# Optimization experiments

Measured on AMD Instinct MI355X. Metric: run time of the kernel, lower is better.

Reference implementation:

```python
import jax, jax.numpy as jnp
import numpy as np

N = 50000      # nodes
E = 800000     # edges
IN = 128       # input feature dim
HID = 64       # out_channels per head
HEADS = 2
OUT = 40       # num classes
SLOPE = 0.2    # leaky relu negative slope
EPS = 1e-16    # PyG softmax denominator epsilon


def _xavier(key, shape):
    fan_out, fan_in = shape[0], shape[1]
    a = float(np.sqrt(6.0 / (fan_in + fan_out)))
    return jax.random.uniform(key, shape, minval=-a, maxval=a, dtype=jnp.float32)


def setup_inputs() -> dict:
    key = jax.random.key(0)
    ks = jax.random.split(key, 16)
    x = jax.random.normal(ks[0], (N, IN), dtype=jnp.float32)
    edge_index = jax.random.randint(ks[1], (2, E), 0, N, dtype=jnp.int64)
    # GAT layer 1: lin_l == lin_r (shared), weight [H*C, in], att [C, H]
    W1 = _xavier(ks[2], (HEADS * HID, IN))
    b1 = jnp.zeros((HEADS * HID,), jnp.float32)
    al1 = _xavier(ks[3], (HID, HEADS))
    ar1 = _xavier(ks[4], (HID, HEADS))
    # GAT layer 2: input dim = heads*hidden
    W2 = _xavier(ks[5], (HEADS * HID, HEADS * HID))
    b2 = jnp.zeros((HEADS * HID,), jnp.float32)
    al2 = _xavier(ks[6], (HID, HEADS))
    ar2 = _xavier(ks[7], (HID, HEADS))
    # post_mp: Linear(heads*hid, hid) -> Linear(hid, out)
    Wp1 = _xavier(ks[8], (HID, HEADS * HID))
    bp1 = jnp.zeros((HID,), jnp.float32)
    Wp2 = _xavier(ks[9], (OUT, HID))
    bp2 = jnp.zeros((OUT,), jnp.float32)
    return dict(x=x, edge_index=edge_index, W1=W1, b1=b1, al1=al1, ar1=ar1,
                W2=W2, b2=b2, al2=al2, ar2=ar2, Wp1=Wp1, bp1=bp1, Wp2=Wp2, bp2=bp2)


def gat_layer(x, edge_index, W, b, att_l, att_r):
    """One GAT layer: shared linear, per-edge leaky-relu scores,
    segment-softmax keyed by destination node, scatter-sum."""
    n = x.shape[0]
    xt = (x @ W.T + b).reshape(n, HEADS, HID)          # [N, H, C] (x_l == x_r)
    alpha_l = jnp.einsum('nhc,ch->nh', xt, att_l)      # [N, H]
    alpha_r = jnp.einsum('nhc,ch->nh', xt, att_r)      # [N, H]
    src, dst = edge_index[0], edge_index[1]            # j = source, i = dest
    e = jax.nn.leaky_relu(alpha_r[dst] + alpha_l[src], SLOPE)   # [E, H]
    # segment softmax over edges grouped by destination node
    seg_max = jax.ops.segment_max(e, dst, num_segments=n)       # [N, H]
    ex = jnp.exp(e - seg_max[dst])
    denom = jax.ops.segment_sum(ex, dst, num_segments=n)        # [N, H]
    alpha = ex / (denom[dst] + EPS)                              # [E, H]
    msg = alpha[:, :, None] * xt[src]                            # [E, H, C]
    out = jax.ops.segment_sum(msg, dst, num_segments=n)          # [N, H, C]
    return out.reshape(n, HEADS * HID)


def reference(x, edge_index, W1, b1, al1, ar1, W2, b2, al2, ar2, Wp1, bp1, Wp2, bp2):
    h = jax.nn.relu(gat_layer(x, edge_index, W1, b1, al1, ar1))
    h = jax.nn.relu(gat_layer(h, edge_index, W2, b2, al2, ar2))
    h = h @ Wp1.T + bp1
    h = h @ Wp2.T + bp2
    return jax.nn.log_softmax(h, axis=1)
```

## Files before the change

kernel.cpp:

```cpp
#include <hip/hip_runtime.h>
#include <hip/hip_fp16.h>
#include <cmath>

#define N_NODES 50000
#define N_EDGES 800000
#define F 128
#define OUT_DIM 40
#define SLOPE 0.2f
#define EPS_DEN 1e-16f

#define BK_SHIFT 7
#define BKSZ 128
#define NBK ((N_NODES + BKSZ - 1) / BKSZ)
#define BK_CAP2 2560
#define SC_CHUNK 2500
#define SC_BLOCKS ((N_EDGES + SC_CHUNK - 1) / SC_CHUNK)
#define GEMM_TILES ((N_NODES + 127) / 128)
#define CB_BLOCKS 33
#define A_BLOCKS (SC_BLOCKS + CB_BLOCKS + GEMM_TILES)
#define SMEM_BYTES 21504
#define POISON ((int)0xAAAAAAAA)

#define AGG_TILE 32
#define AGG_TILES ((N_NODES + AGG_TILE - 1) / AGG_TILE)

typedef _Float16 half8 __attribute__((ext_vector_type(8)));
typedef float floatx4 __attribute__((ext_vector_type(4)));

struct ScatterS { int sd[SC_CHUNK]; short sb[SC_CHUNK]; int h[NBK]; int lofs[NBK]; };
struct GemmS    { __half Ah[128][40]; __half Bh[128][40]; };
static_assert(sizeof(ScatterS) <= SMEM_BYTES, "scatter LDS");
static_assert(sizeof(GemmS)    <= SMEM_BYTES, "gemm LDS");

__device__ __forceinline__ int swz(int row, int chunk) {
  return row * 128 + ((chunk ^ (row & 15)) << 3);
}

__device__ inline float4 load4(const float* p) { return *(const float4*)p; }
__device__ inline float4 load4(const __half* p) {
  uint2 u = *(const uint2*)p;
  float2 a = __half22float2(*(__half2*)&u.x);
  float2 b = __half22float2(*(__half2*)&u.y);
  return make_float4(a.x, a.y, b.x, b.y);
}

__device__ __forceinline__ void scatter_phase(const int* __restrict__ ei,
    int* __restrict__ bcur, int* __restrict__ pairs, int it, int tid, char* smem_) {
  ScatterS* S = (ScatterS*)smem_;
  for (int i = tid; i < NBK; i += 256) S->h[i] = 0;
  __syncthreads();
  int base = it * SC_CHUNK;
  int end = base + SC_CHUNK; if (end > N_EDGES) end = N_EDGES;
  int cnt = end - base;
  for (int e = base + tid; e < end; e += 256) {
    int s = ei[e];
    int d = ei[N_EDGES + e];
    int b = d >> BK_SHIFT;
    S->sd[e - base] = (s << BK_SHIFT) | (d & (BKSZ - 1));
    S->sb[e - base] = (short)b;
    atomicAdd(&S->h[b], 1);
  }
  __syncthreads();
  for (int i = tid; i < NBK; i += 256)
    if (S->h[i]) {
      S->lofs[i] = i * BK_CAP2 + (atomicAdd(&bcur[i], S->h[i]) - POISON);
      S->h[i] = 0;
    }
  __syncthreads();
  for (int i = tid; i < cnt; i += 256) {
    int b = S->sb[i];
    int pos = S->lofs[b] + atomicAdd(&S->h[b], 1);
    pairs[pos] = S->sd[i];
  }
}

__device__ __forceinline__ void combine_phase(const float* __restrict__ Wp1,
    const float* __restrict__ bp1, const float* __restrict__ Wp2,
    const float* __restrict__ bp2, const float* __restrict__ W2,
    __half* __restrict__ Wch, float* __restrict__ bc,
    __half* __restrict__ W2h, int it, int tid) {
  if (it < 24) {
    int idx = it * 256 + tid;
    int o = idx >> 7, k = idx & 127;
    float s = 0.f;
    if (o < OUT_DIM) {
#pragma unroll 8
      for (int j = 0; j < 64; ++j) s += Wp2[o * 64 + j] * Wp1[j * 128 + k];
    }
    Wch[o * 128 + k] = __float2half(s);
  } else if (it == 24) {
    if (tid < 48) {
      int o = tid;
      if (o < OUT_DIM) {
        float s = bp2[o];
        for (int j = 0; j < 64; ++j) s += Wp2[o * 64 + j] * bp1[j];
        bc[o] = s;
      } else {
        bc[o] = -1e30f;
      }
    }
  } else {
    int idx = (it - 25) * 2048 + tid * 8;
    const float* q = W2 + idx;
    float4 w0 = *(const float4*)q, w1 = *(const float4*)(q + 4);
    __half2 g0 = __floats2half2_rn(w0.x, w0.y), g1 = __floats2half2_rn(w0.z, w0.w);
    __half2 g2 = __floats2half2_rn(w1.x, w1.y), g3 = __floats2half2_rn(w1.z, w1.w);
    uint4 qk; qk.x = *(unsigned*)&g0; qk.y = *(unsigned*)&g1;
    qk.z = *(unsigned*)&g2; qk.w = *(unsigned*)&g3;
    *(uint4*)&W2h[idx] = qk;
  }
}

template <typename T>
__device__ __forceinline__ void gemm_phase(const T* __restrict__ A,
    const float* __restrict__ W, const float* __restrict__ b,
    const float* __restrict__ attl, const float* __restrict__ attr,
    __half* __restrict__ Ch, float* __restrict__ al, float* __restrict__ ar,
    int nrows, int tile, int tid, char* smem_) {
  GemmS* S = (GemmS*)smem_;
  int lane = tid & 63, wid = tid >> 6;
  int quad = lane >> 4, col = lane & 15;
  int r0 = tile * 128;
  int rowhalf = wid >> 1, colhalf = wid & 1;
  floatx4 acc[4][4] = {};
  for (int kc = 0; kc < 128; kc += 32) {
    for (int i = tid; i < 512; i += 256) {
      int row = i >> 2, seg = i & 3;
      int gr = r0 + row;
      float4 v0, v1;
      if (gr < nrows) {
        const T* p = A + (size_t)gr * 128 + kc + seg * 8;
        v0 = load4(p); v1 = load4(p + 4);
      } else { v0 = make_float4(0.f,0.f,0.f,0.f); v1 = v0; }
      __half2 h0 = __floats2half2_rn(v0.x, v0.y), h1 = __floats2half2_rn(v0.z, v0.w);
      __half2 h2 = __floats2half2_rn(v1.x, v1.y), h3 = __floats2half2_rn(v1.z, v1.w);
      uint4 pk; pk.x = *(unsigned*)&h0; pk.y = *(unsigned*)&h1;
      pk.z = *(unsigned*)&h2; pk.w = *(unsigned*)&h3;
      *(uint4*)&S->Ah[row][seg * 8] = pk;
      const float* q = W + (size_t)row * 128 + kc + seg * 8;
      float4 w0 = *(const float4*)q, w1 = *(const float4*)(q + 4);
      __half2 g0 = __floats2half2_rn(w0.x, w0.y), g1 = __floats2half2_rn(w0.z, w0.w);
      __half2 g2 = __floats2half2_rn(w1.x, w1.y), g3 = __floats2half2_rn(w1.z, w1.w);
      uint4 qk; qk.x = *(unsigned*)&g0; qk.y = *(unsigned*)&g1;
      qk.z = *(unsigned*)&g2; qk.w = *(unsigned*)&g3;
      *(uint4*)&S->Bh[row][seg * 8] = qk;
    }
    __syncthreads();
    half8 afr[4], bfr[4];
#pragma unroll
    for (int rt = 0; rt < 4; ++rt)
      afr[rt] = *(const half8*)&S->Ah[rowhalf * 64 + rt * 16 + col][quad * 8];
#pragma unroll
    for (int ct = 0; ct < 4; ++ct)
      bfr[ct] = *(const half8*)&S->Bh[colhalf * 64 + ct * 16 + col][quad * 8];
#pragma unroll
    for (int rt = 0; rt < 4; ++rt)
#pragma unroll
      for (int ct = 0; ct < 4; ++ct)
        acc[rt][ct] = __builtin_amdgcn_mfma_f32_16x16x32_f16(afr[rt], bfr[ct],
                                                             acc[rt][ct], 0, 0, 0);
    __syncthreads();
  }
  int head = colhalf;
  float bj[4], wl4[4], wr4[4];
#pragma unroll
  for (int ct = 0; ct < 4; ++ct) {
    int c = ct * 16 + col;
    bj[ct] = b[head * 64 + c];
    wl4[ct] = attl[c * 2 + head];
    wr4[ct] = attr[c * 2 + head];
  }
#pragma unroll
  for (int rt = 0; rt < 4; ++rt) {
#pragma unroll
    for (int reg = 0; reg < 4; ++reg) {
      int gr = r0 + rowhalf * 64 + rt * 16 + quad * 4 + reg;
      bool ok = gr < nrows;
      float pl = 0.f, pr = 0.f;
#pragma unroll
      for (int ct = 0; ct < 4; ++ct) {
        float v = acc[rt][ct][reg] + bj[ct];
        pl += v * wl4[ct]; pr += v * wr4[ct];
        if (ok) Ch[(size_t)gr * F + head * 64 + ct * 16 + col] = __float2half(v);
      }
      pl += __shfl_xor(pl, 1, 64); pr += __shfl_xor(pr, 1, 64);
      pl += __shfl_xor(pl, 2, 64); pr += __shfl_xor(pr, 2, 64);
      pl += __shfl_xor(pl, 4, 64); pr += __shfl_xor(pr, 4, 64);
      pl += __shfl_xor(pl, 8, 64); pr += __shfl_xor(pr, 8, 64);
      if (ok && col == 0) { al[gr * 2 + head] = pl; ar[gr * 2 + head] = pr; }
    }
  }
}

__global__ __launch_bounds__(256) void kernelA(const int* __restrict__ ei,
    int* __restrict__ bcur, int* __restrict__ pairs,
    const float* __restrict__ Wp1, const float* __restrict__ bp1,
    const float* __restrict__ Wp2, const float* __restrict__ bp2,
    const float* __restrict__ W2, __half* __restrict__ Wch,
    float* __restrict__ bc, __half* __restrict__ W2h,
    const float* __restrict__ x, const float* __restrict__ W1,
    const float* __restrict__ b1, const float* __restrict__ al1,
    const float* __restrict__ ar1, __half* __restrict__ xh,
    float* __restrict__ al, float* __restrict__ ar) {
  __shared__ __align__(16) char smem[SMEM_BYTES];
  int bid = blockIdx.x, tid = threadIdx.x;
  if (bid < SC_BLOCKS) {
    scatter_phase(ei, bcur, pairs, bid, tid, smem);
  } else if (bid < SC_BLOCKS + CB_BLOCKS) {
    combine_phase(Wp1, bp1, Wp2, bp2, W2, Wch, bc, W2h, bid - SC_BLOCKS, tid);
  } else {
    gemm_phase<float>(x, W1, b1, al1, ar1, xh, al, ar, N_NODES,
                      bid - SC_BLOCKS - CB_BLOCKS, tid, smem);
  }
}

__global__ __launch_bounds__(512) void local_sort(const int* __restrict__ bcur,
    const int* __restrict__ pairs, int* __restrict__ rowstart,
    int* __restrict__ rowend, int* __restrict__ srcs) {
  __shared__ int buf[BK_CAP2];
  __shared__ int sorted[BK_CAP2];
  __shared__ int hist[BKSZ];
  __shared__ int cur[BKSZ];
  int tid = threadIdx.x;
  int b = blockIdx.x;
  int base = b * BK_CAP2;
  int cnt = bcur[b] - POISON;
  if (cnt > BK_CAP2) cnt = BK_CAP2;
  if (cnt < 0) cnt = 0;
  if (tid < BKSZ) hist[tid] = 0;
  __syncthreads();
  for (int i = tid; i < cnt; i += 512) {
    int p = pairs[base + i];
    buf[i] = p;
    atomicAdd(&hist[p & (BKSZ - 1)], 1);
  }
  __syncthreads();
  if (tid < 64) {
    int lane = tid;
    int carry = 0;
#pragma unroll
    for (int c = 0; c < BKSZ; c += 64) {
      int v = hist[c + lane];
      int x = v;
#pragma unroll
      for (int off = 1; off < 64; off <<= 1) {
        int t = __shfl_up(x, off, 64);
        if (lane >= off) x += t;
      }
      int excl = carry + x - v;
      cur[c + lane] = excl;
      int node = b * BKSZ + c + lane;
      if (node < N_NODES) {
        rowstart[node] = base + excl;
        rowend[node]   = base + excl + v;
      }
      carry += __shfl(x, 63, 64);
    }
  }
  __syncthreads();
  for (int i = tid; i < cnt; i += 512) {
    int p = buf[i];
    int pos = atomicAdd(&cur[p & (BKSZ - 1)], 1);
    sorted[pos] = p >> BK_SHIFT;
  }
  __syncthreads();
  for (int i = tid; i < cnt; i += 512)
    srcs[base + i] = sorted[i];
}

__device__ __forceinline__ void agg_node_to_lds(const int* __restrict__ rowstart,
    const int* __restrict__ rowend, const int* __restrict__ srcs,
    const float* __restrict__ al, const float* __restrict__ ar,
    const __half* __restrict__ xsrc, __half* __restrict__ ldsA,
    float (*ebufw)[64], int* sbufw, int node, int ldsrow, int lane) {
  int g = lane >> 4, q = lane & 15;
  int head = q >> 3;
  if (node >= N_NODES) {
    if (g == 0) {
      uint4 z = {0, 0, 0, 0};
      *(uint4*)&ldsA[swz(ldsrow, q)] = z;
    }
    __builtin_amdgcn_wave_barrier();
    return;
  }
  int start = rowstart[node], end = rowend[node];
  float2 arv = *(const float2*)(ar + (size_t)node * 2);
  float ar0 = arv.x, ar1 = arv.y;
  const float* wrow = &ebufw[head][0];
  const __half* xbase = xsrc + q * 8;
  float acc[8] = {};
  float dl0 = 0.f, dl1 = 0.f;
  for (int c = start; c < end; c += 64) {
    int j = c + lane;
    float e0 = 0.f, e1 = 0.f; int soff = 0;
    if (j < end) {
      int s = srcs[j];
      soff = s << BK_SHIFT;
      float2 a = *(const float2*)(al + (size_t)s * 2);
      float s0 = a.x + ar0; s0 = (s0 > 0.f) ? s0 : SLOPE * s0;
      float s1 = a.y + ar1; s1 = (s1 > 0.f) ? s1 : SLOPE * s1;
      e0 = __expf(s0); e1 = __expf(s1);
    }
    dl0 += e0; dl1 += e1;
    ebufw[0][lane] = e0; ebufw[1][lane] = e1; sbufw[lane] = soff;
    __builtin_amdgcn_wave_barrier();
    int cend = end - c; if (cend > 64) cend = 64;
#pragma unroll 4
    for (int t = 0; t < cend; t += 4) {
      int te = t + g;
      if (te < cend) {
        int so = sbufw[te];
        float w = wrow[te];
        uint4 u = *(const uint4*)(xbase + so);
        const __half2* hh = (const __half2*)&u;
        float2 f0 = __half22float2(hh[0]);
        float2 f1 = __half22float2(hh[1]);
        float2 f2 = __half22float2(hh[2]);
        float2 f3 = __half22float2(hh[3]);
        acc[0] += w * f0.x; acc[1] += w * f0.y;
        acc[2] += w * f1.x; acc[3] += w * f1.y;
        acc[4] += w * f2.x; acc[5] += w * f2.y;
        acc[6] += w * f3.x; acc[7] += w * f3.y;
      }
    }
    __builtin_amdgcn_wave_barrier();
  }
#pragma unroll
  for (int off = 32; off > 0; off >>= 1) {
    dl0 += __shfl_xor(dl0, off, 64);
    dl1 += __shfl_xor(dl1, off, 64);
  }
#pragma unroll
  for (int k = 0; k < 8; ++k) {
    acc[k] += __shfl_xor(acc[k], 16, 64);
    acc[k] += __shfl_xor(acc[k], 32, 64);
  }
  if (g == 0) {
    float d = (head == 0) ? dl0 : dl1;
    float inv = 1.f / (d + EPS_DEN);
    __half2 o0 = __floats2half2_rn(fmaxf(acc[0] * inv, 0.f), fmaxf(acc[1] * inv, 0.f));
    __half2 o1 = __floats2half2_rn(fmaxf(acc[2] * inv, 0.f), fmaxf(acc[3] * inv, 0.f));
    __half2 o2 = __floats2half2_rn(fmaxf(acc[4] * inv, 0.f), fmaxf(acc[5] * inv, 0.f));
    __half2 o3 = __floats2half2_rn(fmaxf(acc[6] * inv, 0.f), fmaxf(acc[7] * inv, 0.f));
    uint4 pack;
    pack.x = *(unsigned*)&o0; pack.y = *(unsigned*)&o1;
    pack.z = *(unsigned*)&o2; pack.w = *(unsigned*)&o3;
    *(uint4*)&ldsA[swz(ldsrow, q)] = pack;
  }
  __builtin_amdgcn_wave_barrier();
}

__global__ __launch_bounds__(256) void fusedB(const int* __restrict__ rowstart,
    const int* __restrict__ rowend, const int* __restrict__ srcs,
    const float* __restrict__ al, const float* __restrict__ ar,
    const __half* __restrict__ xh, const __half* __restrict__ W2h,
    const float* __restrict__ b2,
    const float* __restrict__ attl, const float* __restrict__ attr,
    __half* __restrict__ xh2, float* __restrict__ al2, float* __restrict__ ar2) {
  __shared__ __half Ah[AGG_TILE * 128];
  __shared__ float ebuf[4][2][64];
  __shared__ int   sbuf[4][64];
  int tid = threadIdx.x;
  int wid = tid >> 6, lane = tid & 63;
  int tile = blockIdx.x;
#pragma unroll 1
  for (int r = 0; r < 8; ++r) {
    int ldsrow = r * 4 + wid;
    agg_node_to_lds(rowstart, rowend, srcs, al, ar, xh, Ah,
                    ebuf[wid], sbuf[wid], tile * AGG_TILE + ldsrow, ldsrow, lane);
  }
  __syncthreads();
  int rowg = wid >> 1, colg = wid & 1;
  int quad = lane >> 4, col = lane & 15;
  floatx4 acc[4] = {};
#pragma unroll
  for (int kc4 = 0; kc4 < 4; ++kc4) {
    half8 afr = *(const half8*)&Ah[swz(rowg * 16 + col, (kc4 << 2) | quad)];
#pragma unroll
    for (int ct = 0; ct < 4; ++ct) {
      int brow = colg * 64 + ct * 16 + col;
      half8 bfr = *(const half8*)(W2h + (size_t)brow * 128 + kc4 * 32 + quad * 8);
      acc[ct] = __builtin_amdgcn_mfma_f32_16x16x32_f16(afr, bfr, acc[ct], 0, 0, 0);
    }
  }
  int head = colg;
  float bj[4], wl4[4], wr4[4];
#pragma unroll
  for (int ct = 0; ct < 4; ++ct) {
    int c = ct * 16 + col;
    bj[ct] = b2[head * 64 + c];
    wl4[ct] = attl[c * 2 + head];
    wr4[ct] = attr[c * 2 + head];
  }
#pragma unroll
  for (int reg = 0; reg < 4; ++reg) {
    int gr = tile * AGG_TILE + rowg * 16 + quad * 4 + reg;
    bool ok = gr < N_NODES;
    float pl = 0.f, pr = 0.f;
#pragma unroll
    for (int ct = 0; ct < 4; ++ct) {
      float v = acc[ct][reg] + bj[ct];
      pl += v * wl4[ct]; pr += v * wr4[ct];
      if (ok) xh2[(size_t)gr * F + head * 64 + ct * 16 + col] = __float2half(v);
    }
    pl += __shfl_xor(pl, 1, 64); pr += __shfl_xor(pr, 1, 64);
    pl += __shfl_xor(pl, 2, 64); pr += __shfl_xor(pr, 2, 64);
    pl += __shfl_xor(pl, 4, 64); pr += __shfl_xor(pr, 4, 64);
    pl += __shfl_xor(pl, 8, 64); pr += __shfl_xor(pr, 8, 64);
    if (ok && col == 0) { al2[gr * 2 + head] = pl; ar2[gr * 2 + head] = pr; }
  }
}

__global__ __launch_bounds__(256) void fusedC(const int* __restrict__ rowstart,
    const int* __restrict__ rowend, const int* __restrict__ srcs,
    const float* __restrict__ al2, const float* __restrict__ ar2,
    const __half* __restrict__ xh2,
    const __half* __restrict__ Wch, const float* __restrict__ bc,
    float* __restrict__ out) {
  __shared__ __half Ah[AGG_TILE * 128];
  __shared__ float ebuf[4][2][64];
  __shared__ int   sbuf[4][64];
  int tid = threadIdx.x;
  int wid = tid >> 6, lane = tid & 63;
  int tile = blockIdx.x;
#pragma unroll 1
  for (int r = 0; r < 8; ++r) {
    int ldsrow = r * 4 + wid;
    agg_node_to_lds(rowstart, rowend, srcs, al2, ar2, xh2, Ah,
                    ebuf[wid], sbuf[wid], tile * AGG_TILE + ldsrow, ldsrow, lane);
  }
  __syncthreads();
  if (wid >= 2) return;
  int quad = lane >> 4, col = lane & 15;
  int rbase = wid * 16;
  floatx4 acc[3] = {};
#pragma unroll
  for (int kc4 = 0; kc4 < 4; ++kc4) {
    half8 afr = *(const half8*)&Ah[swz(rbase + col, (kc4 << 2) | quad)];
#pragma unroll
    for (int ct = 0; ct < 3; ++ct) {
      half8 bfr = *(const half8*)(Wch + (size_t)(ct * 16 + col) * 128 + kc4 * 32 + quad * 8);
      acc[ct] = __builtin_amdgcn_mfma_f32_16x16x32_f16(afr, bfr, acc[ct], 0, 0, 0);
    }
  }
  float bcv[3];
#pragma unroll
  for (int ct = 0; ct < 3; ++ct) bcv[ct] = bc[ct * 16 + col];
#pragma unroll
  for (int reg = 0; reg < 4; ++reg) {
    int row = tile * AGG_TILE + rbase + quad * 4 + reg;
    float z[3], m = -INFINITY;
#pragma unroll
    for (int ct = 0; ct < 3; ++ct) { z[ct] = acc[ct][reg] + bcv[ct]; m = fmaxf(m, z[ct]); }
    m = fmaxf(m, __shfl_xor(m, 1, 64));
    m = fmaxf(m, __shfl_xor(m, 2, 64));
    m = fmaxf(m, __shfl_xor(m, 4, 64));
    m = fmaxf(m, __shfl_xor(m, 8, 64));
    float s = 0.f;
#pragma unroll
    for (int ct = 0; ct < 3; ++ct) s += __expf(z[ct] - m);
    s += __shfl_xor(s, 1, 64);
    s += __shfl_xor(s, 2, 64);
    s += __shfl_xor(s, 4, 64);
    s += __shfl_xor(s, 8, 64);
    float ls = logf(s);
    if (row < N_NODES) {
#pragma unroll
      for (int ct = 0; ct < 3; ++ct) {
        int o = ct * 16 + col;
        if (o < OUT_DIM) out[(size_t)row * OUT_DIM + o] = z[ct] - m - ls;
      }
    }
  }
}

extern "C" void kernel_launch(void* const* d_in, const int* in_sizes, int n_in,
                              void* d_out, int out_size, void* d_ws, size_t ws_size,
                              hipStream_t stream) {
  const float* x   = (const float*)d_in[0];
  const int*   ei  = (const int*)d_in[1];
  const float* W1  = (const float*)d_in[2];
  const float* b1  = (const float*)d_in[3];
  const float* al1 = (const float*)d_in[4];
  const float* ar1 = (const float*)d_in[5];
  const float* W2  = (const float*)d_in[6];
  const float* b2  = (const float*)d_in[7];
  const float* al2w= (const float*)d_in[8];
  const float* ar2w= (const float*)d_in[9];
  const float* Wp1 = (const float*)d_in[10];
  const float* bp1 = (const float*)d_in[11];
  const float* Wp2 = (const float*)d_in[12];
  const float* bp2 = (const float*)d_in[13];
  float* out = (float*)d_out;

  float* al    = (float*)d_ws;
  float* ar    = al + (size_t)N_NODES * 2;
  float* al2   = ar + (size_t)N_NODES * 2;
  float* ar2   = al2 + (size_t)N_NODES * 2;
  __half* Wch  = (__half*)(ar2 + (size_t)N_NODES * 2);
  float* bc    = (float*)(Wch + 48 * 128);
  __half* W2h  = (__half*)(bc + 48);
  int* rowstart= (int*)(W2h + 128 * 128);
  int* rowend  = rowstart + N_NODES;
  int* bcur    = rowend + N_NODES;
  int* srcs    = bcur + NBK;
  int* pairs   = srcs + NBK * BK_CAP2;
  uintptr_t pp = ((uintptr_t)(pairs + NBK * BK_CAP2) + 255) & ~(uintptr_t)255;
  __half* xh   = (__half*)pp;
  __half* xh2  = xh + (size_t)N_NODES * F;

  kernelA<<<A_BLOCKS, 256, 0, stream>>>(ei, bcur, pairs, Wp1, bp1, Wp2, bp2,
                                        W2, Wch, bc, W2h, x, W1, b1, al1, ar1,
                                        xh, al, ar);
  local_sort<<<NBK, 512, 0, stream>>>(bcur, pairs, rowstart, rowend, srcs);
  fusedB<<<AGG_TILES, 256, 0, stream>>>(rowstart, rowend, srcs, al, ar, xh,
                                        W2h, b2, al2w, ar2w, xh2, al2, ar2);
  fusedC<<<AGG_TILES, 256, 0, stream>>>(rowstart, rowend, srcs, al2, ar2, xh2,
                                        Wch, bc, out);
}
```

Before: 256.5 us.

## Aggregate per 128-node bucket with precomputed normalized edge weights in LDS

fusedB and fusedC now run one 1024-thread block per 128-node bucket instead of one 256-thread block per 32 nodes. Each block first computes the leaky-relu exp scores for all of the bucket's edges, the per-node softmax denominators and the normalized weights, and keeps them in LDS. To support this, local_sort now stores the packed (src, dst-low) value so the destination can be recovered per edge. The per-node gather then just reads weights and offsets from LDS, which removes the per-chunk wave barriers and the per-wave exp work. In exchange the grid is much smaller with heavier blocks, each block uses far more LDS, and the prologue adds block-wide syncs and a serial per-node denominator loop.

```diff
diff --git a/kernel.cpp b/kernel.cpp
--- a/kernel.cpp
+++ b/kernel.cpp
@@ -20,9 +20,6 @@
 #define A_BLOCKS (SC_BLOCKS + CB_BLOCKS + GEMM_TILES)
 #define SMEM_BYTES 21504
 #define POISON ((int)0xAAAAAAAA)
-
-#define AGG_TILE 32
-#define AGG_TILES ((N_NODES + AGG_TILE - 1) / AGG_TILE)
 
 typedef _Float16 half8 __attribute__((ext_vector_type(8)));
 typedef float floatx4 __attribute__((ext_vector_type(4)));
@@ -261,18 +258,59 @@
   for (int i = tid; i < cnt; i += 512) {
     int p = buf[i];
     int pos = atomicAdd(&cur[p & (BKSZ - 1)], 1);
-    sorted[pos] = p >> BK_SHIFT;
+    sorted[pos] = p;
   }
   __syncthreads();
   for (int i = tid; i < cnt; i += 512)
     srcs[base + i] = sorted[i];
 }
 
-__device__ __forceinline__ void agg_node_to_lds(const int* __restrict__ rowstart,
-    const int* __restrict__ rowend, const int* __restrict__ srcs,
+__device__ __forceinline__ void edge_softmax_prologue(
+    const int* __restrict__ rowstart, const int* __restrict__ rowend,
+    const int* __restrict__ srcs, const int* __restrict__ bcur,
     const float* __restrict__ al, const float* __restrict__ ar,
-    const __half* __restrict__ xsrc, __half* __restrict__ ldsA,
-    float (*ebufw)[64], int* sbufw, int node, int ldsrow, int lane) {
+    float2* __restrict__ wbuf, int* __restrict__ sofs,
+    unsigned char* __restrict__ dlo, float2* __restrict__ inv,
+    int tile, int tid) {
+  int base = tile * BK_CAP2;
+  int cnt = bcur[tile] - POISON;
+  if (cnt > BK_CAP2) cnt = BK_CAP2;
+  if (cnt < 0) cnt = 0;
+  for (int i = tid; i < cnt; i += 1024) {
+    int v = srcs[base + i];
+    int s = v >> BK_SHIFT;
+    int d = v & (BKSZ - 1);
+    sofs[i] = s << BK_SHIFT;
+    dlo[i] = (unsigned char)d;
+    float2 a = *(const float2*)(al + (size_t)s * 2);
+    float2 rr = *(const float2*)(ar + (size_t)(tile * BKSZ + d) * 2);
+    float s0 = a.x + rr.x; s0 = (s0 > 0.f) ? s0 : SLOPE * s0;
+    float s1 = a.y + rr.y; s1 = (s1 > 0.f) ? s1 : SLOPE * s1;
+    wbuf[i] = make_float2(__expf(s0), __expf(s1));
+  }
+  __syncthreads();
+  if (tid < BKSZ) {
+    int node = tile * BKSZ + tid;
+    float d0 = 0.f, d1 = 0.f;
+    if (node < N_NODES) {
+      int ls = rowstart[node] - base, le = rowend[node] - base;
+      for (int j = ls; j < le; ++j) { float2 w = wbuf[j]; d0 += w.x; d1 += w.y; }
+    }
+    inv[tid] = make_float2(1.f / (d0 + EPS_DEN), 1.f / (d1 + EPS_DEN));
+  }
+  __syncthreads();
+  for (int i = tid; i < cnt; i += 1024) {
+    float2 iv = inv[dlo[i]];
+    float2 w = wbuf[i];
+    wbuf[i] = make_float2(w.x * iv.x, w.y * iv.y);
+  }
+  __syncthreads();
+}
+
+__device__ __forceinline__ void agg_node(const int* __restrict__ rowstart,
+    const int* __restrict__ rowend, const __half* __restrict__ xsrc,
+    const float2* __restrict__ wbuf, const int* __restrict__ sofs,
+    __half* __restrict__ ldsA, int base, int node, int ldsrow, int lane) {
   int g = lane >> 4, q = lane & 15;
   int head = q >> 3;
   if (node >= N_NODES) {
@@ -280,55 +318,26 @@
       uint4 z = {0, 0, 0, 0};
       *(uint4*)&ldsA[swz(ldsrow, q)] = z;
     }
-    __builtin_amdgcn_wave_barrier();
     return;
   }
-  int start = rowstart[node], end = rowend[node];
-  float2 arv = *(const float2*)(ar + (size_t)node * 2);
-  float ar0 = arv.x, ar1 = arv.y;
-  const float* wrow = &ebufw[head][0];
+  int ls = rowstart[node] - base, le = rowend[node] - base;
   const __half* xbase = xsrc + q * 8;
   float acc[8] = {};
-  float dl0 = 0.f, dl1 = 0.f;
-  for (int c = start; c < end; c += 64) {
-    int j = c + lane;
-    float e0 = 0.f, e1 = 0.f; int soff = 0;
-    if (j < end) {
-      int s = srcs[j];
-      soff = s << BK_SHIFT;
-      float2 a = *(const float2*)(al + (size_t)s * 2);
-      float s0 = a.x + ar0; s0 = (s0 > 0.f) ? s0 : SLOPE * s0;
-      float s1 = a.y + ar1; s1 = (s1 > 0.f) ? s1 : SLOPE * s1;
-      e0 = __expf(s0); e1 = __expf(s1);
-    }
-    dl0 += e0; dl1 += e1;
-    ebufw[0][lane] = e0; ebufw[1][lane] = e1; sbufw[lane] = soff;
-    __builtin_amdgcn_wave_barrier();
-    int cend = end - c; if (cend > 64) cend = 64;
 #pragma unroll 4
-    for (int t = 0; t < cend; t += 4) {
-      int te = t + g;
-      if (te < cend) {
-        int so = sbufw[te];
-        float w = wrow[te];
-        uint4 u = *(const uint4*)(xbase + so);
-        const __half2* hh = (const __half2*)&u;
-        float2 f0 = __half22float2(hh[0]);
-        float2 f1 = __half22float2(hh[1]);
-        float2 f2 = __half22float2(hh[2]);
-        float2 f3 = __half22float2(hh[3]);
-        acc[0] += w * f0.x; acc[1] += w * f0.y;
-        acc[2] += w * f1.x; acc[3] += w * f1.y;
-        acc[4] += w * f2.x; acc[5] += w * f2.y;
-        acc[6] += w * f3.x; acc[7] += w * f3.y;
-      }
-    }
-    __builtin_amdgcn_wave_barrier();
-  }
-#pragma unroll
-  for (int off = 32; off > 0; off >>= 1) {
-    dl0 += __shfl_xor(dl0, off, 64);
-    dl1 += __shfl_xor(dl1, off, 64);
+  for (int t = ls + g; t < le; t += 4) {
+    int so = sofs[t];
+    float2 wv = wbuf[t];
+    float w = head ? wv.y : wv.x;
+    uint4 u = *(const uint4*)(xbase + so);
+    const __half2* hh = (const __half2*)&u;
+    float2 f0 = __half22float2(hh[0]);
+    float2 f1 = __half22float2(hh[1]);
+    float2 f2 = __half22float2(hh[2]);
+    float2 f3 = __half22float2(hh[3]);
+    acc[0] += w * f0.x; acc[1] += w * f0.y;
+    acc[2] += w * f1.x; acc[3] += w * f1.y;
+    acc[4] += w * f2.x; acc[5] += w * f2.y;
+    acc[6] += w * f3.x; acc[7] += w * f3.y;
   }
 #pragma unroll
   for (int k = 0; k < 8; ++k) {
@@ -336,38 +345,41 @@
     acc[k] += __shfl_xor(acc[k], 32, 64);
   }
   if (g == 0) {
-    float d = (head == 0) ? dl0 : dl1;
-    float inv = 1.f / (d + EPS_DEN);
-    __half2 o0 = __floats2half2_rn(fmaxf(acc[0] * inv, 0.f), fmaxf(acc[1] * inv, 0.f));
-    __half2 o1 = __floats2half2_rn(fmaxf(acc[2] * inv, 0.f), fmaxf(acc[3] * inv, 0.f));
-    __half2 o2 = __floats2half2_rn(fmaxf(acc[4] * inv, 0.f), fmaxf(acc[5] * inv, 0.f));
-    __half2 o3 = __floats2half2_rn(fmaxf(acc[6] * inv, 0.f), fmaxf(acc[7] * inv, 0.f));
+    __half2 o0 = __floats2half2_rn(fmaxf(acc[0], 0.f), fmaxf(acc[1], 0.f));
+    __half2 o1 = __floats2half2_rn(fmaxf(acc[2], 0.f), fmaxf(acc[3], 0.f));
+    __half2 o2 = __floats2half2_rn(fmaxf(acc[4], 0.f), fmaxf(acc[5], 0.f));
+    __half2 o3 = __floats2half2_rn(fmaxf(acc[6], 0.f), fmaxf(acc[7], 0.f));
     uint4 pack;
     pack.x = *(unsigned*)&o0; pack.y = *(unsigned*)&o1;
     pack.z = *(unsigned*)&o2; pack.w = *(unsigned*)&o3;
     *(uint4*)&ldsA[swz(ldsrow, q)] = pack;
   }
-  __builtin_amdgcn_wave_barrier();
-}
-
-__global__ __launch_bounds__(256) void fusedB(const int* __restrict__ rowstart,
+}
+
+__global__ __launch_bounds__(1024) void fusedB(const int* __restrict__ rowstart,
     const int* __restrict__ rowend, const int* __restrict__ srcs,
+    const int* __restrict__ bcur,
     const float* __restrict__ al, const float* __restrict__ ar,
     const __half* __restrict__ xh, const __half* __restrict__ W2h,
     const float* __restrict__ b2,
     const float* __restrict__ attl, const float* __restrict__ attr,
     __half* __restrict__ xh2, float* __restrict__ al2, float* __restrict__ ar2) {
-  __shared__ __half Ah[AGG_TILE * 128];
-  __shared__ float ebuf[4][2][64];
-  __shared__ int   sbuf[4][64];
+  __shared__ __half Ah[128 * 128];
+  __shared__ float2 wbuf[BK_CAP2];
+  __shared__ int    sofs[BK_CAP2];
+  __shared__ float2 inv[BKSZ];
+  __shared__ unsigned char dlo[BK_CAP2];
   int tid = threadIdx.x;
   int wid = tid >> 6, lane = tid & 63;
   int tile = blockIdx.x;
+  int base = tile * BK_CAP2;
+  edge_softmax_prologue(rowstart, rowend, srcs, bcur, al, ar,
+                        wbuf, sofs, dlo, inv, tile, tid);
 #pragma unroll 1
   for (int r = 0; r < 8; ++r) {
-    int ldsrow = r * 4 + wid;
-    agg_node_to_lds(rowstart, rowend, srcs, al, ar, xh, Ah,
-                    ebuf[wid], sbuf[wid], tile * AGG_TILE + ldsrow, ldsrow, lane);
+    int ldsrow = r * 16 + wid;
+    agg_node(rowstart, rowend, xh, wbuf, sofs, Ah, base,
+             tile * BKSZ + ldsrow, ldsrow, lane);
   }
   __syncthreads();
   int rowg = wid >> 1, colg = wid & 1;
@@ -394,7 +406,7 @@
   }
 #pragma unroll
   for (int reg = 0; reg < 4; ++reg) {
-    int gr = tile * AGG_TILE + rowg * 16 + quad * 4 + reg;
+    int gr = tile * BKSZ + rowg * 16 + quad * 4 + reg;
     bool ok = gr < N_NODES;
     float pl = 0.f, pr = 0.f;
 #pragma unroll
@@ -411,26 +423,32 @@
   }
 }
 
-__global__ __launch_bounds__(256) void fusedC(const int* __restrict__ rowstart,
+__global__ __launch_bounds__(1024) void fusedC(const int* __restrict__ rowstart,
     const int* __restrict__ rowend, const int* __restrict__ srcs,
+    const int* __restrict__ bcur,
     const float* __restrict__ al2, const float* __restrict__ ar2,
     const __half* __restrict__ xh2,
     const __half* __restrict__ Wch, const float* __restrict__ bc,
     float* __restrict__ out) {
-  __shared__ __half Ah[AGG_TILE * 128];
-  __shared__ float ebuf[4][2][64];
-  __shared__ int   sbuf[4][64];
+  __shared__ __half Ah[128 * 128];
+  __shared__ float2 wbuf[BK_CAP2];
+  __shared__ int    sofs[BK_CAP2];
+  __shared__ float2 inv[BKSZ];
+  __shared__ unsigned char dlo[BK_CAP2];
   int tid = threadIdx.x;
   int wid = tid >> 6, lane = tid & 63;
   int tile = blockIdx.x;
+  int base = tile * BK_CAP2;
+  edge_softmax_prologue(rowstart, rowend, srcs, bcur, al2, ar2,
+                        wbuf, sofs, dlo, inv, tile, tid);
 #pragma unroll 1
   for (int r = 0; r < 8; ++r) {
-    int ldsrow = r * 4 + wid;
-    agg_node_to_lds(rowstart, rowend, srcs, al2, ar2, xh2, Ah,
-                    ebuf[wid], sbuf[wid], tile * AGG_TILE + ldsrow, ldsrow, lane);
-  }
-  __syncthreads();
-  if (wid >= 2) return;
+    int ldsrow = r * 16 + wid;
+    agg_node(rowstart, rowend, xh2, wbuf, sofs, Ah, base,
+             tile * BKSZ + ldsrow, ldsrow, lane);
+  }
+  __syncthreads();
+  if (wid >= 8) return;
   int quad = lane >> 4, col = lane & 15;
   int rbase = wid * 16;
   floatx4 acc[3] = {};
@@ -448,7 +466,7 @@
   for (int ct = 0; ct < 3; ++ct) bcv[ct] = bc[ct * 16 + col];
 #pragma unroll
   for (int reg = 0; reg < 4; ++reg) {
-    int row = tile * AGG_TILE + rbase + quad * 4 + reg;
+    int row = tile * BKSZ + rbase + quad * 4 + reg;
     float z[3], m = -INFINITY;
 #pragma unroll
     for (int ct = 0; ct < 3; ++ct) { z[ct] = acc[ct][reg] + bcv[ct]; m = fmaxf(m, z[ct]); }
@@ -513,8 +531,8 @@
                                         W2, Wch, bc, W2h, x, W1, b1, al1, ar1,
                                         xh, al, ar);
   local_sort<<<NBK, 512, 0, stream>>>(bcur, pairs, rowstart, rowend, srcs);
-  fusedB<<<AGG_TILES, 256, 0, stream>>>(rowstart, rowend, srcs, al, ar, xh,
-                                        W2h, b2, al2w, ar2w, xh2, al2, ar2);
-  fusedC<<<AGG_TILES, 256, 0, stream>>>(rowstart, rowend, srcs, al2, ar2, xh2,
-                                        Wch, bc, out);
-}
+  fusedB<<<NBK, 1024, 0, stream>>>(rowstart, rowend, srcs, bcur, al, ar, xh,
+                                   W2h, b2, al2w, ar2w, xh2, al2, ar2);
+  fusedC<<<NBK, 1024, 0, stream>>>(rowstart, rowend, srcs, bcur, al2, ar2, xh2,
+                                   Wch, bc, out);
+}
```

New measurement: 240.8 us. 6.1% less time.
